# Kernel optimization log

Hardware: AMD Instinct MI355X
Metric: run time of the kernel (lower is better)

## Reference

```python
import jax, jax.numpy as jnp
import numpy as np
from jax import lax

B, M, D_IN, EPG = 512, 64, 32, 512   # pairs, nodes/graph, one_hot_dim, edges/graph
GCN_SIZES = [64, 32, 16]
K = 5                                 # conv kernel (odd -> 'same' pad 2)
LIN = [12288, 256, 64]                # 12288 = 3 sim-mats * 16 ch * 16 * 16


def _edges(seed):
    # random intra-graph edges: per-graph node ids in [0,M) offset by graph id
    r = np.random.default_rng(seed)
    off = np.repeat(np.arange(B, dtype=np.int64) * M, EPG)
    s = r.integers(0, M, B * EPG) + off
    d = r.integers(0, M, B * EPG) + off
    return jnp.asarray(s, jnp.int32), jnp.asarray(d, jnp.int32)


def setup_inputs():
    key = jax.random.key(0)
    ks = iter(jax.random.split(key, 32))
    def nrm(shape, fan_in):
        return jax.random.normal(next(ks), shape, jnp.float32) * (fan_in ** -0.5)
    src_q, dst_q = _edges(1)
    src_c, dst_c = _edges(2)
    return dict(
        x_q=jax.random.normal(next(ks), (B * M, D_IN), jnp.float32),
        x_c=jax.random.normal(next(ks), (B * M, D_IN), jnp.float32),
        src_q=src_q, dst_q=dst_q, src_c=src_c, dst_c=dst_c,
        Wg0=nrm((D_IN, 64), D_IN), bg0=jnp.zeros((64,), jnp.float32),
        Wg1=nrm((64, 32), 64), bg1=jnp.zeros((32,), jnp.float32),
        Wg2=nrm((32, 16), 32), bg2=jnp.zeros((16,), jnp.float32),
        cw0=nrm((3, 8, 1, K, K), K * K), cb0=jnp.zeros((3, 8), jnp.float32),
        cw1=nrm((3, 16, 8, K, K), 8 * K * K), cb1=jnp.zeros((3, 16), jnp.float32),
        Wl0=nrm((LIN[0], LIN[1]), LIN[0]), bl0=jnp.zeros((LIN[1],), jnp.float32),
        Wl1=nrm((LIN[1], LIN[2]), LIN[1]), bl1=jnp.zeros((LIN[2],), jnp.float32),
        Wsc=nrm((LIN[2], 1), LIN[2]), bsc=jnp.zeros((1,), jnp.float32),
    )


def _gcn_pass(x, src, dst, Ws, bs):
    # PyG GCNConv: x @ W, add self loops, symmetric deg^-1/2 normalization,
    # scatter-add to dst, + bias. Eval mode (dropout off).
    N = x.shape[0]
    sl = jnp.arange(N, dtype=src.dtype)
    s = jnp.concatenate([src, sl])
    d = jnp.concatenate([dst, sl])
    deg = jax.ops.segment_sum(jnp.ones(s.shape, x.dtype), d, num_segments=N)
    dinv = lax.rsqrt(deg)
    norm = (dinv[s] * dinv[d])[:, None]
    feats = []
    h = x
    for i in range(len(Ws)):
        h = h @ Ws[i]
        h = jax.ops.segment_sum(h[s] * norm, d, num_segments=N) + bs[i]
        feats.append(h)
        if i < len(Ws) - 1:
            h = jax.nn.relu(h)
    return feats


def _conv(x, w, b):
    y = lax.conv_general_dilated(x, w, (1, 1), ((K // 2, K // 2), (K // 2, K // 2)),
                                 dimension_numbers=('NCHW', 'OIHW', 'NCHW'))
    return y + b[None, :, None, None]


def _maxpool2(x):
    # torch: ZeroPad2d((0,1,0,1)) then MaxPool2d(2, 2)
    xp = jnp.pad(x, ((0, 0), (0, 0), (0, 1), (0, 1)))
    return lax.reduce_window(xp, -jnp.inf, lax.max, (1, 1, 2, 2), (1, 1, 2, 2), 'VALID')


def _forward(x_q, x_c, src_q, dst_q, src_c, dst_c,
             Wg0, bg0, Wg1, bg1, Wg2, bg2,
             cw0, cb0, cw1, cb1, Wl0, bl0, Wl1, bl1, Wsc, bsc):
    Ws, bs = [Wg0, Wg1, Wg2], [bg0, bg1, bg2]
    qf = _gcn_pass(x_q, src_q, dst_q, Ws, bs)
    cf = _gcn_pass(x_c, src_c, dst_c, Ws, bs)
    # all graphs have exactly M nodes -> pad_sequence is a reshape; sim is [B,1,M,M]
    feats = [jnp.einsum('bmd,bnd->bmn', qf[i].reshape(B, M, -1),
                        cf[i].reshape(B, M, -1))[:, None] for i in range(3)]
    cws, cbs = [cw0, cw1], [cb0, cb1]
    for l in range(2):
        feats = [_maxpool2(jax.nn.relu(_conv(feats[i], cws[l][i], cbs[l][i])))
                 for i in range(3)]
    h = jnp.concatenate(feats, axis=1).reshape(-1, LIN[0])
    h = jax.nn.relu(h @ Wl0 + bl0)
    h = jax.nn.relu(h @ Wl1 + bl1)
    return jax.nn.sigmoid(h @ Wsc + bsc).reshape(-1)


def reference(x_q, x_c, src_q, dst_q, src_c, dst_c,
              Wg0, bg0, Wg1, bg1, Wg2, bg2,
              cw0, cb0, cw1, cb1, Wl0, bl0, Wl1, bl1, Wsc, bsc):
    return _forward(x_q, x_c, src_q, dst_q, src_c, dst_c,
                    Wg0, bg0, Wg1, bg1, Wg2, bg2,
                    cw0, cb0, cw1, cb1, Wl0, bl0, Wl1, bl1, Wsc, bsc)
```

## Files before the change

kernel.cpp:

```cpp
#include <hip/hip_runtime.h>
#include <math.h>

#define NB 512
#define MM 64
#define EPGc 512

typedef __attribute__((ext_vector_type(8))) short s16x8;
typedef __attribute__((ext_vector_type(4))) float f32x4;

__device__ __forceinline__ unsigned short f2bf(float f) {
  union { float f; unsigned int u; } c; c.f = f;
  unsigned int u = c.u;
  return (unsigned short)((u + 0x7FFFu + ((u >> 16) & 1u)) >> 16);
}
__device__ __forceinline__ float bf2f(unsigned short h) {
  union { unsigned int u; float f; } c; c.u = ((unsigned int)h) << 16;
  return c.f;
}

template<int Fin, int Fout, bool RELU>
__device__ __forceinline__ void gcn_layer_mfma(
    const unsigned short* __restrict__ WT, const float* __restrict__ bias,
    unsigned short* hbuf, unsigned short* stT, const unsigned short* Ab,
    unsigned short* __restrict__ outG, int g, int tid)
{
  const int lane = tid & 63, w = tid >> 6;
  const int c = lane & 15, q = lane >> 4;
  constexpr int NT = Fout / 16;
  constexpr int KS = Fin / 32;

#pragma unroll
  for (int nt = 0; nt < NT; ++nt) {
    f32x4 acc = {0.f, 0.f, 0.f, 0.f};
#pragma unroll
    for (int ks = 0; ks < KS; ++ks) {
      s16x8 a = *reinterpret_cast<const s16x8*>(hbuf + (w * 16 + c) * 72 + ks * 32 + q * 8);
      s16x8 b = *reinterpret_cast<const s16x8*>(WT + (nt * 16 + c) * Fin + ks * 32 + q * 8);
      acc = __builtin_amdgcn_mfma_f32_16x16x32_bf16(a, b, acc, 0, 0, 0);
    }
    unsigned int w0 = (unsigned int)f2bf(acc[0]) | ((unsigned int)f2bf(acc[1]) << 16);
    unsigned int w1 = (unsigned int)f2bf(acc[2]) | ((unsigned int)f2bf(acc[3]) << 16);
    *reinterpret_cast<uint2*>(stT + (nt * 16 + c) * 72 + w * 16 + q * 4) = make_uint2(w0, w1);
  }
  __syncthreads();

#pragma unroll
  for (int mt = 0; mt < NT; ++mt) {
    f32x4 acc = {0.f, 0.f, 0.f, 0.f};
#pragma unroll
    for (int ks = 0; ks < 2; ++ks) {
      s16x8 a = *reinterpret_cast<const s16x8*>(stT + (mt * 16 + c) * 72 + ks * 32 + q * 8);
      s16x8 b = *reinterpret_cast<const s16x8*>(Ab + (w * 16 + c) * 72 + ks * 32 + q * 8);
      acc = __builtin_amdgcn_mfma_f32_16x16x32_bf16(a, b, acc, 0, 0, 0);
    }
    const int node = w * 16 + c, f0 = mt * 16 + q * 4;
    unsigned short pk[4], pr[4];
#pragma unroll
    for (int r = 0; r < 4; ++r) {
      float v = acc[r] + bias[f0 + r];
      pk[r] = f2bf(v);
      pr[r] = f2bf(fmaxf(v, 0.f));
    }
    *reinterpret_cast<uint2*>(outG + (size_t)(g * MM + node) * Fout + f0) =
        make_uint2((unsigned int)pk[0] | ((unsigned int)pk[1] << 16),
                   (unsigned int)pk[2] | ((unsigned int)pk[3] << 16));
    if (RELU)
      *reinterpret_cast<uint2*>(hbuf + node * 72 + f0) =
          make_uint2((unsigned int)pr[0] | ((unsigned int)pr[1] << 16),
                     (unsigned int)pr[2] | ((unsigned int)pr[3] << 16));
  }
  __syncthreads();
}

__global__ __launch_bounds__(256) void gcn_kernel(
    const float* __restrict__ xq, const float* __restrict__ xc,
    const int* __restrict__ srcq, const int* __restrict__ dstq,
    const int* __restrict__ srcc, const int* __restrict__ dstc,
    const unsigned short* __restrict__ WgT,
    const float* __restrict__ bg0, const float* __restrict__ bg1, const float* __restrict__ bg2,
    unsigned short* __restrict__ qf0, unsigned short* __restrict__ qf1,
    unsigned short* __restrict__ qf2, unsigned short* __restrict__ cf0,
    unsigned short* __restrict__ cf1, unsigned short* __restrict__ cf2)
{
  __shared__ __align__(16) unsigned short smem[13824];
  __shared__ float sDinv[MM];
  __shared__ int sDeg[MM];
  unsigned short* hbuf = smem;
  unsigned short* stT  = smem + 4608;
  unsigned short* Ab   = smem + 9216;
  float* sAf = reinterpret_cast<float*>(smem);

  const int g = blockIdx.x;
  const int which = blockIdx.y;
  const float* x = which ? xc : xq;
  const int* src = which ? srcc : srcq;
  const int* dst = which ? dstc : dstq;
  unsigned short* f0p = which ? cf0 : qf0;
  unsigned short* f1p = which ? cf1 : qf1;
  unsigned short* f2p = which ? cf2 : qf2;
  const int tid = threadIdx.x;

  for (int i = tid; i < 64 * 68; i += 256) sAf[i] = 0.f;
  if (tid < MM) sDeg[tid] = 1;
  __syncthreads();
  for (int e = tid; e < EPGc; e += 256)
    atomicAdd(&sDeg[dst[g * EPGc + e] - g * MM], 1);
  __syncthreads();
  if (tid < MM) sDinv[tid] = rsqrtf((float)sDeg[tid]);
  __syncthreads();
  for (int e = tid; e < EPGc; e += 256) {
    int s = src[g * EPGc + e] - g * MM;
    int d = dst[g * EPGc + e] - g * MM;
    atomicAdd(&sAf[d * 68 + s], sDinv[s] * sDinv[d]);
  }
  if (tid < MM) atomicAdd(&sAf[tid * 68 + tid], sDinv[tid] * sDinv[tid]);
  __syncthreads();
  for (int i = tid; i < 4096; i += 256) {
    int r = i >> 6, s = i & 63;
    Ab[r * 72 + s] = f2bf(sAf[r * 68 + s]);
  }
  __syncthreads();
  {
    const float* xs = x + (size_t)g * 2048 + tid * 8;
    float4 v0 = *reinterpret_cast<const float4*>(xs);
    float4 v1 = *reinterpret_cast<const float4*>(xs + 4);
    s16x8 p;
    p[0] = (short)f2bf(v0.x); p[1] = (short)f2bf(v0.y); p[2] = (short)f2bf(v0.z); p[3] = (short)f2bf(v0.w);
    p[4] = (short)f2bf(v1.x); p[5] = (short)f2bf(v1.y); p[6] = (short)f2bf(v1.z); p[7] = (short)f2bf(v1.w);
    int node = tid >> 2, k = (tid & 3) * 8;
    *reinterpret_cast<s16x8*>(hbuf + node * 72 + k) = p;
  }
  __syncthreads();

  gcn_layer_mfma<32, 64, true >(WgT,        bg0, hbuf, stT, Ab, f0p, g, tid);
  gcn_layer_mfma<64, 32, true >(WgT + 2048, bg1, hbuf, stT, Ab, f1p, g, tid);
  gcn_layer_mfma<32, 16, false>(WgT + 4096, bg2, hbuf, stT, Ab, f2p, g, tid);
}

__global__ __launch_bounds__(256) void prep_misc(
    const float* __restrict__ cw1, const float* __restrict__ cw0,
    const float* __restrict__ Wg0, const float* __restrict__ Wg1, const float* __restrict__ Wg2,
    const float* __restrict__ Wl0,
    unsigned short* __restrict__ packA, unsigned short* __restrict__ packW1,
    unsigned short* __restrict__ WgT, unsigned short* __restrict__ WT)
{
  __shared__ float tile[64][65];
  const int b = blockIdx.x, t = threadIdx.x;
  if (b < 42) {
    int i = b * 256 + t;
    if (i < 10752) {
      int j = i & 7, l = (i >> 3) & 63, g = (i >> 9) % 7, lvl = i / 3584;
      int oc = l & 15, sg = l >> 4;
      int s = g * 4 + sg;
      float v = 0.f;
      if (s < 25) v = cw1[((size_t)(lvl * 16 + oc) * 8 + j) * 25 + s];
      packA[i] = f2bf(v);
    }
    return;
  }
  if (b < 54) {
    int i = (b - 42) * 256 + t;
    if (i < 3072) {
      int j = i & 7, lane = (i >> 3) & 63, gg = (i >> 9) & 1, lvl = i >> 10;
      int m = lane & 15, q = lane >> 4;
      int u = gg * 4 + q;
      int oc = m & 7;
      float v = 0.f;
      if (u < 5) {
        if (m < 8) { if (j < 5) v = cw0[((size_t)(lvl * 8 + oc)) * 25 + u * 5 + j]; }
        else       { if (j >= 1 && j <= 5) v = cw0[((size_t)(lvl * 8 + oc)) * 25 + u * 5 + (j - 1)]; }
      }
      packW1[i] = f2bf(v);
    }
    return;
  }
  if (b < 72) {
    int i = (b - 54) * 256 + t;
    if (i < 2048) {
      int n = i >> 5, k = i & 31;
      WgT[i] = f2bf(Wg0[k * 64 + n]);
    } else if (i < 4096) {
      int j = i - 2048, n = j >> 6, k = j & 63;
      WgT[i] = f2bf(Wg1[k * 32 + n]);
    } else if (i < 4608) {
      int j = i - 4096, n = j >> 5, k = j & 31;
      WgT[i] = f2bf(Wg2[k * 16 + n]);
    }
    return;
  }
  {
    int bb = b - 72;
    const int kb = (bb % 192) * 64;
    const int nb = (bb / 192) * 64;
#pragma unroll
    for (int i = 0; i < 16; ++i) {
      int idx = i * 256 + t, kk = idx >> 6, nn = idx & 63;
      tile[kk][nn] = Wl0[(size_t)(kb + kk) * 256 + nb + nn];
    }
    __syncthreads();
#pragma unroll
    for (int i = 0; i < 16; ++i) {
      int idx = i * 256 + t, nn = idx >> 6, kk = idx & 63;
      WT[(size_t)(nb + nn) * 12288 + kb + kk] = f2bf(tile[kk][nn]);
    }
  }
}

template<int F>
__device__ __forceinline__ void sim_mfma(const unsigned short* __restrict__ qf,
    const unsigned short* __restrict__ cf, unsigned short* qbf, unsigned short* cbf,
    unsigned short* cp, int g, int tid)
{
  constexpr int SQ = (F == 16) ? 40 : F + 8;
  {
    unsigned int* z = reinterpret_cast<unsigned int*>(cp);
    for (int i = tid; i < 2880; i += 256) z[i] = 0u;
  }
  for (int i = tid; i < 64 * F / 8; i += 256) {
    int row = (i * 8) / F, k = (i * 8) % F;
    s16x8 qv = *reinterpret_cast<const s16x8*>(qf + (size_t)g * 64 * F + i * 8);
    s16x8 cv = *reinterpret_cast<const s16x8*>(cf + (size_t)g * 64 * F + i * 8);
    *reinterpret_cast<s16x8*>(qbf + row * SQ + k) = qv;
    *reinterpret_cast<s16x8*>(cbf + row * SQ + k) = cv;
  }
  if (F == 16) {
    for (int i = tid; i < 128; i += 256) {
      int row = i >> 1, h = (i & 1) * 8;
      s16x8 zz = {0, 0, 0, 0, 0, 0, 0, 0};
      *reinterpret_cast<s16x8*>(qbf + row * SQ + 16 + h) = zz;
      *reinterpret_cast<s16x8*>(cbf + row * SQ + 16 + h) = zz;
    }
  }
  __syncthreads();

  const int lane = tid & 63, wave = tid >> 6;
  const int c = lane & 15, q = lane >> 4;
  constexpr int NK = (F == 64) ? 2 : 1;

  f32x4 acc[4];
#pragma unroll
  for (int nt = 0; nt < 4; ++nt) acc[nt] = (f32x4){0.f, 0.f, 0.f, 0.f};
#pragma unroll
  for (int ks = 0; ks < NK; ++ks) {
    s16x8 af = *reinterpret_cast<const s16x8*>(qbf + (wave * 16 + c) * SQ + ks * 32 + q * 8);
#pragma unroll
    for (int nt = 0; nt < 4; ++nt) {
      s16x8 bf = *reinterpret_cast<const s16x8*>(cbf + (nt * 16 + c) * SQ + ks * 32 + q * 8);
      acc[nt] = __builtin_amdgcn_mfma_f32_16x16x32_bf16(af, bf, acc[nt], 0, 0, 0);
    }
  }
#pragma unroll
  for (int nt = 0; nt < 4; ++nt)
#pragma unroll
    for (int r = 0; r < 4; ++r)
      cp[(wave * 16 + q * 4 + r + 2) * 80 + nt * 16 + c + 2] = f2bf(acc[nt][r]);
  __syncthreads();
}

__device__ __forceinline__ void conv1_mfma(const unsigned short* cp,
    unsigned short* p1u, const unsigned short* __restrict__ packW1,
    const float* __restrict__ cb0, int lvl, int tid)
{
  const int lane = tid & 63, wave = tid >> 6;
  const int c = lane & 15, q = lane >> 4;

  for (int h = tid; h < 272; h += 256) {
    int r, cc;
    if (h < 72)       { r = h / 36;             cc = h % 36; }
    else if (h < 144) { r = 34 + (h - 72) / 36; cc = (h - 72) % 36; }
    else { int z = h - 144; r = 2 + (z >> 2); int wq = z & 3; cc = (wq < 2) ? wq : 32 + wq; }
    s16x8 zz = {0, 0, 0, 0, 0, 0, 0, 0};
    *reinterpret_cast<s16x8*>(p1u + (r * 36 + cc) * 8) = zz;
  }

  s16x8 aw0 = *reinterpret_cast<const s16x8*>(packW1 + ((size_t)(lvl * 2 + 0) * 64 + lane) * 8);
  s16x8 aw1 = *reinterpret_cast<const s16x8*>(packW1 + ((size_t)(lvl * 2 + 1) * 64 + lane) * 8);
  float bias[4];
#pragma unroll
  for (int r = 0; r < 4; ++r) bias[r] = cb0[lvl * 8 + (q & 1) * 4 + r];

  const unsigned int* b32 = reinterpret_cast<const unsigned int*>(cp);

  for (int pp = 0; pp < 8; ++pp) {
    const int Y = wave * 8 + pp;
    const int y0 = 2 * Y;
#pragma unroll
    for (int Xi = 0; Xi < 2; ++Xi) {
      const int P = Xi * 16 + c;
      const int col = P;
      const int r00 = (y0 + q) * 40 + col;
      const int r01 = (y0 + 4 + q) * 40 + col;
      const int r10 = (y0 + 1 + q) * 40 + col;
      const int r11 = (y0 + 5 + q) * 40 + col;
      union { unsigned int w[4]; s16x8 v; } f00, f01, f10, f11;
#pragma unroll
      for (int k = 0; k < 4; ++k) {
        f00.w[k] = b32[r00 + k]; f01.w[k] = b32[r01 + k];
        f10.w[k] = b32[r10 + k]; f11.w[k] = b32[r11 + k];
      }
      f32x4 a0 = {0.f, 0.f, 0.f, 0.f}, a1 = {0.f, 0.f, 0.f, 0.f};
      a0 = __builtin_amdgcn_mfma_f32_16x16x32_bf16(aw0, f00.v, a0, 0, 0, 0);
      a0 = __builtin_amdgcn_mfma_f32_16x16x32_bf16(aw1, f01.v, a0, 0, 0, 0);
      a1 = __builtin_amdgcn_mfma_f32_16x16x32_bf16(aw0, f10.v, a1, 0, 0, 0);
      a1 = __builtin_amdgcn_mfma_f32_16x16x32_bf16(aw1, f11.v, a1, 0, 0, 0);
      float pv[4];
#pragma unroll
      for (int r = 0; r < 4; ++r) {
        float vm = fmaxf(a0[r], a1[r]);
        float hp = fmaxf(vm, __shfl_xor(vm, 32));
        pv[r] = fmaxf(hp + bias[r], 0.f);
      }
      if (q < 2) {
        unsigned short pk[4];
#pragma unroll
        for (int r = 0; r < 4; ++r) pk[r] = f2bf(pv[r]);
        unsigned int w0 = (unsigned int)pk[0] | ((unsigned int)pk[1] << 16);
        unsigned int w1 = (unsigned int)pk[2] | ((unsigned int)pk[3] << 16);
        *reinterpret_cast<uint2*>(p1u + (((Y + 2) * 36) + (P + 2)) * 8 + q * 4) =
            make_uint2(w0, w1);
      }
    }
  }
  __syncthreads();
}

__global__ __launch_bounds__(256) void simconv_kernel(
    const unsigned short* __restrict__ qf0, const unsigned short* __restrict__ qf1,
    const unsigned short* __restrict__ qf2, const unsigned short* __restrict__ cf0,
    const unsigned short* __restrict__ cf1, const unsigned short* __restrict__ cf2,
    const float* __restrict__ cb0, const float* __restrict__ cb1,
    const unsigned short* __restrict__ packA, const unsigned short* __restrict__ packW1,
    unsigned short* __restrict__ hcat)
{
  __shared__ __align__(16) unsigned short smem[16128];
  unsigned short* qbf = smem;
  unsigned short* cbf = smem + 4608;
  unsigned short* p1u = smem;
  unsigned short* cp  = smem + 10368;

  const int g = blockIdx.x, lvl = blockIdx.y, tid = threadIdx.x;

  if (lvl == 0)      sim_mfma<64>(qf0, cf0, qbf, cbf, cp, g, tid);
  else if (lvl == 1) sim_mfma<32>(qf1, cf1, qbf, cbf, cp, g, tid);
  else               sim_mfma<16>(qf2, cf2, qbf, cbf, cp, g, tid);

  conv1_mfma(cp, p1u, packW1, cb0, lvl, tid);

  {
    const int lane = tid & 63, wave = tid >> 6;
    const int col = lane & 15, q = lane >> 4;

    s16x8 afr[7];
#pragma unroll
    for (int gg = 0; gg < 7; ++gg)
      afr[gg] = *reinterpret_cast<const s16x8*>(packA + ((size_t)(lvl * 7 + gg) * 64 + lane) * 8);

    int off[7];
#pragma unroll
    for (int gg = 0; gg < 7; ++gg) {
      int s = gg * 4 + q; if (s > 24) s = 24;
      off[gg] = (s / 5) * 288 + (s % 5) * 8;
    }
    float bias2[4];
#pragma unroll
    for (int r = 0; r < 4; ++r) bias2[r] = cb1[lvl * 16 + q * 4 + r];

    for (int pq = 0; pq < 4; ++pq) {
      const int py = wave * 4 + pq;
#pragma unroll
      for (int h = 0; h < 2; ++h) {
        const int base0 = (2 * py) * 288 + h * 128 + col * 8;
        const int base1 = base0 + 288;
        f32x4 a0 = {0.f, 0.f, 0.f, 0.f}, a1 = {0.f, 0.f, 0.f, 0.f};
#pragma unroll
        for (int gg = 0; gg < 7; ++gg) {
          s16x8 b0 = *reinterpret_cast<const s16x8*>(p1u + base0 + off[gg]);
          a0 = __builtin_amdgcn_mfma_f32_16x16x32_bf16(afr[gg], b0, a0, 0, 0, 0);
          s16x8 b1 = *reinterpret_cast<const s16x8*>(p1u + base1 + off[gg]);
          a1 = __builtin_amdgcn_mfma_f32_16x16x32_bf16(afr[gg], b1, a1, 0, 0, 0);
        }
        float val[4];
#pragma unroll
        for (int r = 0; r < 4; ++r) {
          float vm = fmaxf(a0[r], a1[r]);
          float hp = fmaxf(vm, __shfl_xor(vm, 1));
          val[r] = fmaxf(hp + bias2[r], 0.f);
        }
        if ((col & 1) == 0) {
          int px = h * 8 + (col >> 1);
#pragma unroll
          for (int r = 0; r < 4; ++r)
            hcat[((size_t)g * 48 + lvl * 16 + q * 4 + r) * 256 + py * 16 + px] = f2bf(val[r]);
        }
      }
    }
  }
}

__global__ __launch_bounds__(256) void lin0_kernel(
    const unsigned short* __restrict__ A, const unsigned short* __restrict__ WT,
    float* __restrict__ part)
{
  __shared__ __align__(16) unsigned short sAb[64 * 72];
  __shared__ __align__(16) unsigned short sBb[64 * 72];
  const int rb = blockIdx.x * 64;
  const int cb = blockIdx.y * 64;
  const int k0 = blockIdx.z * 768;
  const int tid = threadIdx.x;
  const int lane = tid & 63, wave = tid >> 6;
  const int wm = wave >> 1, wn = wave & 1;
  const int c = lane & 15, kg = lane >> 4;
  const int srow = tid >> 2;
  const int skq  = (tid & 3) * 16;

  f32x4 acc[2][2];
#pragma unroll
  for (int i = 0; i < 2; ++i)
#pragma unroll
    for (int j = 0; j < 2; ++j) acc[i][j] = (f32x4){0.f, 0.f, 0.f, 0.f};

  for (int kt = 0; kt < 768; kt += 64) {
    {
      const unsigned short* src = A + (size_t)(rb + srow) * 12288 + k0 + kt + skq;
      s16x8 a0 = *reinterpret_cast<const s16x8*>(src);
      s16x8 a1 = *reinterpret_cast<const s16x8*>(src + 8);
      *reinterpret_cast<s16x8*>(sAb + srow * 72 + skq)     = a0;
      *reinterpret_cast<s16x8*>(sAb + srow * 72 + skq + 8) = a1;
    }
    {
      const unsigned short* src = WT + (size_t)(cb + srow) * 12288 + k0 + kt + skq;
      s16x8 w0 = *reinterpret_cast<const s16x8*>(src);
      s16x8 w1 = *reinterpret_cast<const s16x8*>(src + 8);
      *reinterpret_cast<s16x8*>(sBb + srow * 72 + skq)     = w0;
      *reinterpret_cast<s16x8*>(sBb + srow * 72 + skq + 8) = w1;
    }
    __syncthreads();

#pragma unroll
    for (int kb = 0; kb < 64; kb += 32) {
      s16x8 a0 = *reinterpret_cast<const s16x8*>(sAb + (wm * 32 +  0 + c) * 72 + kb + kg * 8);
      s16x8 a1 = *reinterpret_cast<const s16x8*>(sAb + (wm * 32 + 16 + c) * 72 + kb + kg * 8);
      s16x8 b0 = *reinterpret_cast<const s16x8*>(sBb + (wn * 32 +  0 + c) * 72 + kb + kg * 8);
      s16x8 b1 = *reinterpret_cast<const s16x8*>(sBb + (wn * 32 + 16 + c) * 72 + kb + kg * 8);
      acc[0][0] = __builtin_amdgcn_mfma_f32_16x16x32_bf16(a0, b0, acc[0][0], 0, 0, 0);
      acc[0][1] = __builtin_amdgcn_mfma_f32_16x16x32_bf16(a0, b1, acc[0][1], 0, 0, 0);
      acc[1][0] = __builtin_amdgcn_mfma_f32_16x16x32_bf16(a1, b0, acc[1][0], 0, 0, 0);
      acc[1][1] = __builtin_amdgcn_mfma_f32_16x16x32_bf16(a1, b1, acc[1][1], 0, 0, 0);
    }
    __syncthreads();
  }

  float* dstp = part + (size_t)blockIdx.z * 512 * 256;
#pragma unroll
  for (int i = 0; i < 2; ++i)
#pragma unroll
    for (int j = 0; j < 2; ++j)
#pragma unroll
      for (int r = 0; r < 4; ++r) {
        int row = rb + wm * 32 + i * 16 + kg * 4 + r;
        int col = cb + wn * 32 + j * 16 + c;
        dstp[(size_t)row * 256 + col] = acc[i][j][r];
      }
}

__global__ __launch_bounds__(64) void head_kernel(
    const float* __restrict__ part, const float* __restrict__ bl0,
    const float* __restrict__ Wl1, const float* __restrict__ bl1,
    const float* __restrict__ Wsc, const float* __restrict__ bsc, float* __restrict__ out)
{
  __shared__ float sr[256];
  const int b = blockIdx.x, j = threadIdx.x;
  {
    float4 s = *reinterpret_cast<const float4*>(bl0 + j * 4);
#pragma unroll
    for (int z = 0; z < 16; ++z) {
      float4 p = *reinterpret_cast<const float4*>(part + ((size_t)z * 512 + b) * 256 + j * 4);
      s.x += p.x; s.y += p.y; s.z += p.z; s.w += p.w;
    }
    sr[j * 4 + 0] = fmaxf(s.x, 0.f);
    sr[j * 4 + 1] = fmaxf(s.y, 0.f);
    sr[j * 4 + 2] = fmaxf(s.z, 0.f);
    sr[j * 4 + 3] = fmaxf(s.w, 0.f);
  }
  __syncthreads();
  float acc = bl1[j];
  for (int k = 0; k < 256; ++k) acc = fmaf(sr[k], Wl1[k * 64 + j], acc);
  float v = fmaxf(acc, 0.f) * Wsc[j];
#pragma unroll
  for (int off = 32; off > 0; off >>= 1) v += __shfl_down(v, off);
  if (j == 0) out[b] = 1.f / (1.f + expf(-(v + bsc[0])));
}

extern "C" void kernel_launch(void* const* d_in, const int* in_sizes, int n_in,
                              void* d_out, int out_size, void* d_ws, size_t ws_size,
                              hipStream_t stream)
{
  (void)in_sizes; (void)n_in; (void)out_size; (void)ws_size;
  const float* x_q = (const float*)d_in[0];
  const float* x_c = (const float*)d_in[1];
  const int*   src_q = (const int*)d_in[2];
  const int*   dst_q = (const int*)d_in[3];
  const int*   src_c = (const int*)d_in[4];
  const int*   dst_c = (const int*)d_in[5];
  const float* Wg0 = (const float*)d_in[6];
  const float* bg0 = (const float*)d_in[7];
  const float* Wg1 = (const float*)d_in[8];
  const float* bg1 = (const float*)d_in[9];
  const float* Wg2 = (const float*)d_in[10];
  const float* bg2 = (const float*)d_in[11];
  const float* cw0 = (const float*)d_in[12];
  const float* cb0 = (const float*)d_in[13];
  const float* cw1 = (const float*)d_in[14];
  const float* cb1 = (const float*)d_in[15];
  const float* Wl0 = (const float*)d_in[16];
  const float* bl0 = (const float*)d_in[17];
  const float* Wl1 = (const float*)d_in[18];
  const float* bl1 = (const float*)d_in[19];
  const float* Wsc = (const float*)d_in[20];
  const float* bsc = (const float*)d_in[21];
  float* out = (float*)d_out;

  float* ws = (float*)d_ws;
  unsigned short* qf0 = (unsigned short*)ws; ws += (size_t)NB * MM * 64 / 2;
  unsigned short* qf1 = (unsigned short*)ws; ws += (size_t)NB * MM * 32 / 2;
  unsigned short* qf2 = (unsigned short*)ws; ws += (size_t)NB * MM * 16 / 2;
  unsigned short* cf0 = (unsigned short*)ws; ws += (size_t)NB * MM * 64 / 2;
  unsigned short* cf1 = (unsigned short*)ws; ws += (size_t)NB * MM * 32 / 2;
  unsigned short* cf2 = (unsigned short*)ws; ws += (size_t)NB * MM * 16 / 2;
  unsigned short* hcat = (unsigned short*)ws; ws += (size_t)NB * 48 * 256 / 2;
  float* part = ws; ws += (size_t)16 * 512 * 256;
  unsigned short* packA  = (unsigned short*)ws; ws += 5376;
  unsigned short* packW1 = (unsigned short*)ws; ws += 1536;
  unsigned short* WgT    = (unsigned short*)ws; ws += 2304;
  unsigned short* WT = (unsigned short*)ws; ws += (size_t)256 * 12288 / 2;

  prep_misc<<<840, 256, 0, stream>>>(cw1, cw0, Wg0, Wg1, Wg2, Wl0,
                                     packA, packW1, WgT, WT);

  gcn_kernel<<<dim3(NB, 2), 256, 0, stream>>>(x_q, x_c, src_q, dst_q, src_c, dst_c,
      WgT, bg0, bg1, bg2, qf0, qf1, qf2, cf0, cf1, cf2);

  simconv_kernel<<<dim3(NB, 3), 256, 0, stream>>>(qf0, qf1, qf2, cf0, cf1, cf2,
      cb0, cb1, packA, packW1, hcat);

  lin0_kernel<<<dim3(8, 4, 16), 256, 0, stream>>>(hcat, WT, part);
  head_kernel<<<NB, 64, 0, stream>>>(part, bl0, Wl1, bl1, Wsc, bsc, out);
}
```

Measured before the change: 78.68 us.

## Load sim-matrix MFMA operands directly from global and add shifted LDS copy for aligned conv reads

The similarity step now loads q/c feature fragments straight from global memory into MFMA operands, dropping the LDS staging and its barrier. It also writes the padded similarity map twice: once at the normal offset and once shifted by two elements. Odd lanes in conv1 can then read 8-byte aligned pairs with uint2 loads instead of four scalar dword loads. This costs extra LDS (smem grows from 16128 to 21888 shorts), which may reduce occupancy, plus doubled zeroing and stores.

```diff
diff --git a/kernel.cpp b/kernel.cpp
--- a/kernel.cpp
+++ b/kernel.cpp
@@ -208,56 +208,51 @@
 
 template<int F>
 __device__ __forceinline__ void sim_mfma(const unsigned short* __restrict__ qf,
-    const unsigned short* __restrict__ cf, unsigned short* qbf, unsigned short* cbf,
-    unsigned short* cp, int g, int tid)
-{
-  constexpr int SQ = (F == 16) ? 40 : F + 8;
+    const unsigned short* __restrict__ cf, unsigned short* cp0, unsigned short* cpS,
+    int g, int tid)
+{
   {
-    unsigned int* z = reinterpret_cast<unsigned int*>(cp);
-    for (int i = tid; i < 2880; i += 256) z[i] = 0u;
-  }
-  for (int i = tid; i < 64 * F / 8; i += 256) {
-    int row = (i * 8) / F, k = (i * 8) % F;
-    s16x8 qv = *reinterpret_cast<const s16x8*>(qf + (size_t)g * 64 * F + i * 8);
-    s16x8 cv = *reinterpret_cast<const s16x8*>(cf + (size_t)g * 64 * F + i * 8);
-    *reinterpret_cast<s16x8*>(qbf + row * SQ + k) = qv;
-    *reinterpret_cast<s16x8*>(cbf + row * SQ + k) = cv;
-  }
-  if (F == 16) {
-    for (int i = tid; i < 128; i += 256) {
-      int row = i >> 1, h = (i & 1) * 8;
-      s16x8 zz = {0, 0, 0, 0, 0, 0, 0, 0};
-      *reinterpret_cast<s16x8*>(qbf + row * SQ + 16 + h) = zz;
-      *reinterpret_cast<s16x8*>(cbf + row * SQ + 16 + h) = zz;
-    }
-  }
-  __syncthreads();
+    unsigned int* z = reinterpret_cast<unsigned int*>(cp0);
+    for (int i = tid; i < 5760; i += 256) z[i] = 0u;
+  }
 
   const int lane = tid & 63, wave = tid >> 6;
   const int c = lane & 15, q = lane >> 4;
   constexpr int NK = (F == 64) ? 2 : 1;
+  const unsigned short* qg = qf + (size_t)g * 64 * F;
+  const unsigned short* cg = cf + (size_t)g * 64 * F;
+  const bool zlane = (F == 16) && (q >= 2);
+  const s16x8 zz8 = {0, 0, 0, 0, 0, 0, 0, 0};
 
   f32x4 acc[4];
 #pragma unroll
   for (int nt = 0; nt < 4; ++nt) acc[nt] = (f32x4){0.f, 0.f, 0.f, 0.f};
 #pragma unroll
   for (int ks = 0; ks < NK; ++ks) {
-    s16x8 af = *reinterpret_cast<const s16x8*>(qbf + (wave * 16 + c) * SQ + ks * 32 + q * 8);
+    s16x8 af = zlane ? zz8
+        : *reinterpret_cast<const s16x8*>(qg + (wave * 16 + c) * F + ks * 32 + q * 8);
 #pragma unroll
     for (int nt = 0; nt < 4; ++nt) {
-      s16x8 bf = *reinterpret_cast<const s16x8*>(cbf + (nt * 16 + c) * SQ + ks * 32 + q * 8);
+      s16x8 bf = zlane ? zz8
+          : *reinterpret_cast<const s16x8*>(cg + (nt * 16 + c) * F + ks * 32 + q * 8);
       acc[nt] = __builtin_amdgcn_mfma_f32_16x16x32_bf16(af, bf, acc[nt], 0, 0, 0);
     }
   }
+  __syncthreads();
+
 #pragma unroll
   for (int nt = 0; nt < 4; ++nt)
 #pragma unroll
-    for (int r = 0; r < 4; ++r)
-      cp[(wave * 16 + q * 4 + r + 2) * 80 + nt * 16 + c + 2] = f2bf(acc[nt][r]);
-  __syncthreads();
-}
-
-__device__ __forceinline__ void conv1_mfma(const unsigned short* cp,
+    for (int r = 0; r < 4; ++r) {
+      unsigned short bv = f2bf(acc[nt][r]);
+      int off = (wave * 16 + q * 4 + r + 2) * 80 + nt * 16 + c + 2;
+      cp0[off] = bv;
+      cpS[off - 2] = bv;
+    }
+  __syncthreads();
+}
+
+__device__ __forceinline__ void conv1_mfma(const unsigned short* cp0, const unsigned short* cpS,
     unsigned short* p1u, const unsigned short* __restrict__ packW1,
     const float* __restrict__ cb0, int lvl, int tid)
 {
@@ -279,7 +274,8 @@
 #pragma unroll
   for (int r = 0; r < 4; ++r) bias[r] = cb0[lvl * 8 + (q & 1) * 4 + r];
 
-  const unsigned int* b32 = reinterpret_cast<const unsigned int*>(cp);
+  const int p = c & 1;
+  const unsigned int* bsel = reinterpret_cast<const unsigned int*>(p ? cpS : cp0);
 
   for (int pp = 0; pp < 8; ++pp) {
     const int Y = wave * 8 + pp;
@@ -287,17 +283,20 @@
 #pragma unroll
     for (int Xi = 0; Xi < 2; ++Xi) {
       const int P = Xi * 16 + c;
-      const int col = P;
-      const int r00 = (y0 + q) * 40 + col;
-      const int r01 = (y0 + 4 + q) * 40 + col;
-      const int r10 = (y0 + 1 + q) * 40 + col;
-      const int r11 = (y0 + 5 + q) * 40 + col;
-      union { unsigned int w[4]; s16x8 v; } f00, f01, f10, f11;
-#pragma unroll
-      for (int k = 0; k < 4; ++k) {
-        f00.w[k] = b32[r00 + k]; f01.w[k] = b32[r01 + k];
-        f10.w[k] = b32[r10 + k]; f11.w[k] = b32[r11 + k];
-      }
+      const int dbase = P - p;
+      const int r00 = (y0 + q) * 40 + dbase;
+      const int r01 = (y0 + 4 + q) * 40 + dbase;
+      const int r10 = (y0 + 1 + q) * 40 + dbase;
+      const int r11 = (y0 + 5 + q) * 40 + dbase;
+      union { uint2 d[2]; s16x8 v; } f00, f01, f10, f11;
+      f00.d[0] = *reinterpret_cast<const uint2*>(bsel + r00);
+      f00.d[1] = *reinterpret_cast<const uint2*>(bsel + r00 + 2);
+      f01.d[0] = *reinterpret_cast<const uint2*>(bsel + r01);
+      f01.d[1] = *reinterpret_cast<const uint2*>(bsel + r01 + 2);
+      f10.d[0] = *reinterpret_cast<const uint2*>(bsel + r10);
+      f10.d[1] = *reinterpret_cast<const uint2*>(bsel + r10 + 2);
+      f11.d[0] = *reinterpret_cast<const uint2*>(bsel + r11);
+      f11.d[1] = *reinterpret_cast<const uint2*>(bsel + r11 + 2);
       f32x4 a0 = {0.f, 0.f, 0.f, 0.f}, a1 = {0.f, 0.f, 0.f, 0.f};
       a0 = __builtin_amdgcn_mfma_f32_16x16x32_bf16(aw0, f00.v, a0, 0, 0, 0);
       a0 = __builtin_amdgcn_mfma_f32_16x16x32_bf16(aw1, f01.v, a0, 0, 0, 0);
@@ -332,19 +331,18 @@
     const unsigned short* __restrict__ packA, const unsigned short* __restrict__ packW1,
     unsigned short* __restrict__ hcat)
 {
-  __shared__ __align__(16) unsigned short smem[16128];
-  unsigned short* qbf = smem;
-  unsigned short* cbf = smem + 4608;
+  __shared__ __align__(16) unsigned short smem[21888];
   unsigned short* p1u = smem;
-  unsigned short* cp  = smem + 10368;
+  unsigned short* cp0 = smem + 10368;
+  unsigned short* cpS = smem + 16128;
 
   const int g = blockIdx.x, lvl = blockIdx.y, tid = threadIdx.x;
 
-  if (lvl == 0)      sim_mfma<64>(qf0, cf0, qbf, cbf, cp, g, tid);
-  else if (lvl == 1) sim_mfma<32>(qf1, cf1, qbf, cbf, cp, g, tid);
-  else               sim_mfma<16>(qf2, cf2, qbf, cbf, cp, g, tid);
-
-  conv1_mfma(cp, p1u, packW1, cb0, lvl, tid);
+  if (lvl == 0)      sim_mfma<64>(qf0, cf0, cp0, cpS, g, tid);
+  else if (lvl == 1) sim_mfma<32>(qf1, cf1, cp0, cpS, g, tid);
+  else               sim_mfma<16>(qf2, cf2, cp0, cpS, g, tid);
+
+  conv1_mfma(cp0, cpS, p1u, packW1, cb0, lvl, tid);
 
   {
     const int lane = tid & 63, wave = tid >> 6;
```

Result: slower. 81.49 us (+3.6%).
